# Optimization experiments

Measured on AMD Instinct MI355X. Metric: run time of the kernel, lower is better.

Reference implementation:

```python
import jax, jax.numpy as jnp
import numpy as np

NB, BS = 64, 128          # num_blocks, block_size (W.shape[1]=8192)
TAU = 3.0                 # iteration=0 -> start temperature
SINKHORN_ITERS = 5


def sinkhorn(logits, tau=TAU, iters=SINKHORN_ITERS):
    P = jax.nn.softmax(logits / tau, axis=-1)
    for _ in range(iters):
        P = P / P.sum(axis=-1, keepdims=True)
        P = P / P.sum(axis=-2, keepdims=True)
    return P


def _lsa_min(cost):
    """Hungarian (Jonker-Volgenant / e-maxx) min-cost assignment on a square
    matrix; returns col index for each row. Matches scipy.linear_sum_assignment."""
    cost = np.asarray(cost, np.float64)
    n = cost.shape[0]
    INF = 1e18
    u = np.zeros(n + 1)
    v = np.zeros(n + 1)
    p = np.zeros(n + 1, np.int64)  # p[j] = row (1-based) assigned to column j
    for i in range(1, n + 1):
        p[0] = i
        j0 = 0
        minv = np.full(n + 1, INF)
        used = np.zeros(n + 1, bool)
        way = np.zeros(n + 1, np.int64)
        while True:
            used[j0] = True
            i0 = p[j0]
            free = ~used[1:]
            cur = cost[i0 - 1] - u[i0] - v[1:]
            upd = free & (cur < minv[1:])
            minv[1:][upd] = cur[upd]
            way[1:][upd] = j0
            masked = np.where(free, minv[1:], INF)
            j1 = int(np.argmin(masked)) + 1
            delta = masked[j1 - 1]
            u[p[used]] += delta
            v[used] -= delta
            minv[1:][free] -= delta
            j0 = j1
            if p[j0] == 0:
                break
        while j0 != 0:  # augment along alternating path
            j1 = way[j0]
            p[j0] = p[j1]
            j0 = j1
    col_of_row = np.empty(n, np.int64)
    col_of_row[p[1:] - 1] = np.arange(n)
    return col_of_row


def hungarian_hard(P_np):
    """Per-block hard permutation maximizing P (i.e. min cost = -P)."""
    nb, bs, _ = P_np.shape
    hard = np.zeros((nb, bs, bs), np.float32)
    rows = np.arange(bs)
    for b in range(nb):
        hard[b, rows, _lsa_min(-P_np[b])] = 1.0
    return hard


def _soft_perm(weight, scale):
    w = weight * scale
    # torch: weight.data.clamp_(-1, 1)  -> straight-through clamp
    w = w + jax.lax.stop_gradient(jnp.clip(w, -1.0, 1.0) - w)
    return sinkhorn(w)


def _assemble(blocks):
    nb, bs, _ = blocks.shape
    G = nb * bs
    idx = jnp.arange(nb)
    out = jnp.zeros((nb, bs, nb, bs), blocks.dtype)
    out = out.at[idx, :, idx, :].set(blocks)
    return out.reshape(G, G)


def setup_inputs() -> dict:
    key = jax.random.key(0)
    k1, _ = jax.random.split(key)
    bound = 1.0 / np.sqrt(BS)
    weight = jax.random.uniform(k1, (NB, BS, BS), jnp.float32, -bound, bound)
    scale = jnp.asarray(np.sqrt(BS), jnp.float32)
    return {"weight": weight, "scale": scale}


def reference(weight, scale):
    P = _soft_perm(weight, scale)                       # (NB, BS, BS)
    hard = jnp.asarray(hungarian_hard(np.asarray(P)))   # constant hard perms
    # STE: (hard - P).detach() + P  ==  hard + (P - stop_grad(P))
    blocks = hard + (P - jax.lax.stop_gradient(P))
    return _assemble(blocks)                             # (8192, 8192)
```

## Files before the change

kernel.cpp:

```cpp
#include <hip/hip_runtime.h>
#include <hip/hip_bf16.h>

#define NBLK 64
#define BS   128
#define GSZ  8192

__device__ __forceinline__ int rl32(int v, int sl) {
    return __builtin_amdgcn_readlane(v, sl);
}
__device__ __forceinline__ double rl64(double v, int sl) {
    union { double d; unsigned u[2]; } a; a.d = v;
    unsigned lo = (unsigned)__builtin_amdgcn_readlane((int)a.u[0], sl);
    unsigned hi = (unsigned)__builtin_amdgcn_readlane((int)a.u[1], sl);
    union { unsigned u[2]; double d; } r; r.u[0] = lo; r.u[1] = hi;
    return r.d;
}
__device__ __forceinline__ unsigned long long pkey(double m, int col) {
    union { double d; unsigned long long u; } a; a.d = m;
    unsigned long long x = a.u;
    x = (x >> 63) ? ~x : (x | 0x8000000000000000ull);
    return (x & ~0xFFull) | (unsigned long long)(unsigned)col;
}

__device__ __forceinline__ unsigned wave_min_u32_dpp(unsigned x) {
    x = min(x, (unsigned)__builtin_amdgcn_update_dpp((int)x, (int)x, 0x111, 0xf, 0xf, false));
    x = min(x, (unsigned)__builtin_amdgcn_update_dpp((int)x, (int)x, 0x112, 0xf, 0xf, false));
    x = min(x, (unsigned)__builtin_amdgcn_update_dpp((int)x, (int)x, 0x114, 0xf, 0xf, false));
    x = min(x, (unsigned)__builtin_amdgcn_update_dpp((int)x, (int)x, 0x118, 0xf, 0xf, false));
    x = min(x, (unsigned)__builtin_amdgcn_update_dpp((int)x, (int)x, 0x142, 0xa, 0xf, false));
    x = min(x, (unsigned)__builtin_amdgcn_update_dpp((int)x, (int)x, 0x143, 0xc, 0xf, false));
    return (unsigned)__builtin_amdgcn_readlane((int)x, 63);
}

__device__ __forceinline__ unsigned long long wave_min_key(unsigned long long k) {
    unsigned hi = (unsigned)(k >> 32);
    unsigned lo = (unsigned)k;
    unsigned mh = wave_min_u32_dpp(hi);
    unsigned long long msk = __ballot(hi == mh);
    unsigned lo_cand = (hi == mh) ? lo : 0xFFFFFFFFu;
    unsigned ml;
    if (__popcll(msk) == 1) {
        ml = (unsigned)__builtin_amdgcn_readlane((int)lo_cand, (int)__builtin_ctzll(msk));
    } else {
        ml = wave_min_u32_dpp(lo_cand);
    }
    return ((unsigned long long)mh << 32) | ml;
}

__global__ __launch_bounds__(256) void k_fused(const float* __restrict__ w,
                                               const float* __restrict__ scale_p,
                                               float* __restrict__ out) {
    __shared__ float M[BS][BS + 1];
    __shared__ int   rowasg[BS];
    float* Mf = &M[0][0];

    const int b = blockIdx.x;
    const int t = threadIdx.x;
    const float scale = *scale_p;

    if (t < BS) {
        for (int r = 0; r < BS; ++r) {
            float x = w[((size_t)b * BS + r) * BS + t] * scale;
            x = fminf(fmaxf(x, -1.0f), 1.0f);
            M[r][t] = x / 3.0f;
        }
    }
    __syncthreads();
    if (t < BS) {
        float mx = M[t][0];
        for (int c = 1; c < BS; ++c) mx = fmaxf(mx, M[t][c]);
        float s = 0.0f;
        for (int c = 0; c < BS; ++c) { float e = expf(M[t][c] - mx); M[t][c] = e; s += e; }
        float rs = 1.0f / s;
        for (int c = 0; c < BS; ++c) M[t][c] *= rs;
    }
    __syncthreads();
    for (int it = 0; it < 5; ++it) {
        if (t < BS) {
            float s = 0.0f;
            for (int c = 0; c < BS; ++c) s += M[t][c];
            float rs = 1.0f / s;
            for (int c = 0; c < BS; ++c) M[t][c] *= rs;
        }
        __syncthreads();
        if (t < BS) {
            float s = 0.0f;
            for (int r = 0; r < BS; ++r) s += M[r][t];
            float rs = 1.0f / s;
            for (int r = 0; r < BS; ++r) M[r][t] *= rs;
        }
        __syncthreads();
    }

    int pA = 0, pB = 0;

    if (t >= 64) {
        const int l = t - 64;
        float4 z = make_float4(0.f, 0.f, 0.f, 0.f);
        float4* o4 = reinterpret_cast<float4*>(out + (size_t)b * BS * GSZ);
        for (int k = l; k < BS * GSZ / 4; k += 192) o4[k] = z;
    } else {
        const int jAcol = t + 1, jBcol = t + 65;
        double uA = 0.0, uB = 0.0, vA, vB;

        {
            float cmA = Mf[t];      int raA = 0;
            float cmB = Mf[t + 64]; int raB = 0;
            for (int r = 1; r < BS; ++r) {
                float xA = Mf[r * (BS + 1) + t];
                if (xA > cmA) { cmA = xA; raA = r; }
                float xB = Mf[r * (BS + 1) + t + 64];
                if (xB > cmB) { cmB = xB; raB = r; }
            }
            vA = -(double)cmA; vB = -(double)cmB;
            rowasg[t] = 0x7FFFFFFF; rowasg[t + 64] = 0x7FFFFFFF;
            __threadfence_block();
            atomicMin(&rowasg[raA], jAcol);
            atomicMin(&rowasg[raB], jBcol);
            __threadfence_block();
            pA = (rowasg[raA] == jAcol) ? raA + 1 : 0;
            pB = (rowasg[raB] == jBcol) ? raB + 1 : 0;
        }

        unsigned long long un0 = __ballot(rowasg[t]      == 0x7FFFFFFF);
        unsigned long long un1 = __ballot(rowasg[t + 64] == 0x7FFFFFFF);

        for (int steps = 0; (un0 | un1) && steps < 512; ++steps) {
            int i;
            if (un0) i = __builtin_ctzll(un0) + 1;
            else     i = __builtin_ctzll(un1) + 65;

            double dA = -(double)Mf[(i - 1) * (BS + 1) + t]      - vA;
            double dB = -(double)Mf[(i - 1) * (BS + 1) + t + 64] - vB;
            unsigned long long kA = pkey(dA, jAcol), kB = pkey(dB, jBcol);

            unsigned long long k1 = wave_min_key(kA < kB ? kA : kB);
            const int  j1  = (int)(k1 & 0xFFull);
            const int  sl1 = (j1 - 1) & 63;
            const bool h1  = j1 > 64;
            double u1 = rl64(h1 ? dB : dA, sl1);

            unsigned long long kA2 = (jAcol == j1) ? ~0ull : kA;
            unsigned long long kB2 = (jBcol == j1) ? ~0ull : kB;
            unsigned long long k2 = wave_min_key(kA2 < kB2 ? kA2 : kB2);
            const int  j2  = (int)(k2 & 0xFFull);
            const int  sl2 = (j2 - 1) & 63;
            const bool h2  = j2 > 64;
            double u2 = rl64(h2 ? dB : dA, sl2);

            int i1 = rl32(h1 ? pB : pA, sl1);

            if (t == sl1) {
                if (h1) { pB = i; uB = u2; if (u1 < u2) vB -= (u2 - u1); }
                else    { pA = i; uA = u2; if (u1 < u2) vA -= (u2 - u1); }
            }
            if (i <= 64) un0 &= ~(1ull << (i - 1)); else un1 &= ~(1ull << (i - 65));
            if (i1 > 0) {
                if (i1 <= 64) un0 |= 1ull << (i1 - 1); else un1 |= 1ull << (i1 - 65);
            }
        }

        while (un0 | un1) {
            int i;
            if (un0) { int r = __builtin_ctzll(un0); un0 &= un0 - 1; i = r + 1; }
            else     { int r = __builtin_ctzll(un1); un1 &= un1 - 1; i = r + 65; }

            bool usedA = false, usedB = false;
            double mA = 1e18, mB = 1e18, SUM = 0.0;
            unsigned long long keyA = ~0ull, keyB = ~0ull;
            int wayA = 0, wayB = 0;
            int i0 = i, j0 = 0;
            double ui0 = 0.0;

            for (int guard = 0; guard <= BS + 2; ++guard) {
                float cA = Mf[(i0 - 1) * (BS + 1) + t];
                float cB = Mf[(i0 - 1) * (BS + 1) + t + 64];
                if (!usedA) {
                    double nd = (-(double)cA - ui0 - vA) + SUM;
                    if (nd < mA) { mA = nd; wayA = j0; keyA = pkey(nd, jAcol); }
                }
                if (!usedB) {
                    double nd = (-(double)cB - ui0 - vB) + SUM;
                    if (nd < mB) { mB = nd; wayB = j0; keyB = pkey(nd, jBcol); }
                }
                unsigned long long kw = wave_min_key(keyA < keyB ? keyA : keyB);
                const int  j1 = (int)(kw & 0xFFull);
                const int  sl = (j1 - 1) & 63;
                const bool hb = j1 > 64;

                double m_win = rl64(hb ? mB : mA, sl);
                double delta = m_win - SUM;
                SUM += delta;
                if (usedA) { uA += delta; vA -= delta; }
                if (usedB) { uB += delta; vB -= delta; }

                int pj = rl32(hb ? pB : pA, sl);
                j0 = j1;
                if (pj == 0) break;
                ui0 = rl64(hb ? uB : uA, sl);
                i0 = pj;
                if (!hb && t == sl) { usedA = true; keyA = ~0ull; }
                if ( hb && t == sl) { usedB = true; keyB = ~0ull; }
            }

            int jc = j0;
            for (int guard = 0; guard <= BS + 2; ++guard) {
                const int  slc = (jc - 1) & 63;
                const bool hc  = jc > 64;
                int jp = rl32(hc ? wayB : wayA, slc);
                int nprow; double nu;
                if (jp == 0) { nprow = i; nu = SUM; }
                else {
                    const int  slp = (jp - 1) & 63;
                    const bool hp  = jp > 64;
                    nprow = rl32(hp ? pB : pA, slp);
                    nu    = rl64(hp ? uB : uA, slp);
                }
                if (!hc) { if (t == slc) { pA = nprow; uA = nu; } }
                else     { if (t == slc) { pB = nprow; uB = nu; } }
                if (jp == 0) break;
                jc = jp;
            }
        }
    }

    __syncthreads();

    if (t < 64) {
        const size_t base = (size_t)b * BS;
        if (pA >= 1) out[(base + (size_t)(pA - 1)) * GSZ + base + t]      = 1.0f;
        if (pB >= 1) out[(base + (size_t)(pB - 1)) * GSZ + base + t + 64] = 1.0f;
    }
}

extern "C" void kernel_launch(void* const* d_in, const int* in_sizes, int n_in,
                              void* d_out, int out_size, void* d_ws, size_t ws_size,
                              hipStream_t stream) {
    const float* w     = (const float*)d_in[0];
    const float* scale = (const float*)d_in[1];
    float* out = (float*)d_out;
    k_fused<<<NBLK, 256, 0, stream>>>(w, scale, out);
}
```

Before: 780.3 us.

## Replace auction preprocessing and per-row augmentation with multi-source Dijkstra augmentation

Drops the Jonker-Volgenant-style reduction-transfer preprocessing loop and the single-source-per-row augmentation loop. Each phase now seeds the shortest-path search from all unassigned rows at once (an unrolled-by-4 scan over the unassigned set), finds the nearest free column, and augments back to whichever source row produced it. This is meant to cut wave-wide reductions and dependent readlane chains per augmentation. The cost is an O(unassigned x columns) seeding scan every phase, and the change in tie-breaking could pick a different optimal assignment than the reference when costs tie.

```diff
diff --git a/kernel.cpp b/kernel.cpp
--- a/kernel.cpp
+++ b/kernel.cpp
@@ -125,92 +125,84 @@
         unsigned long long un0 = __ballot(rowasg[t]      == 0x7FFFFFFF);
         unsigned long long un1 = __ballot(rowasg[t + 64] == 0x7FFFFFFF);
 
-        for (int steps = 0; (un0 | un1) && steps < 512; ++steps) {
-            int i;
-            if (un0) i = __builtin_ctzll(un0) + 1;
-            else     i = __builtin_ctzll(un1) + 65;
-
-            double dA = -(double)Mf[(i - 1) * (BS + 1) + t]      - vA;
-            double dB = -(double)Mf[(i - 1) * (BS + 1) + t + 64] - vB;
-            unsigned long long kA = pkey(dA, jAcol), kB = pkey(dB, jBcol);
-
-            unsigned long long k1 = wave_min_key(kA < kB ? kA : kB);
-            const int  j1  = (int)(k1 & 0xFFull);
-            const int  sl1 = (j1 - 1) & 63;
-            const bool h1  = j1 > 64;
-            double u1 = rl64(h1 ? dB : dA, sl1);
-
-            unsigned long long kA2 = (jAcol == j1) ? ~0ull : kA;
-            unsigned long long kB2 = (jBcol == j1) ? ~0ull : kB;
-            unsigned long long k2 = wave_min_key(kA2 < kB2 ? kA2 : kB2);
-            const int  j2  = (int)(k2 & 0xFFull);
-            const int  sl2 = (j2 - 1) & 63;
-            const bool h2  = j2 > 64;
-            double u2 = rl64(h2 ? dB : dA, sl2);
-
-            int i1 = rl32(h1 ? pB : pA, sl1);
-
-            if (t == sl1) {
-                if (h1) { pB = i; uB = u2; if (u1 < u2) vB -= (u2 - u1); }
-                else    { pA = i; uA = u2; if (u1 < u2) vA -= (u2 - u1); }
-            }
-            if (i <= 64) un0 &= ~(1ull << (i - 1)); else un1 &= ~(1ull << (i - 65));
-            if (i1 > 0) {
-                if (i1 <= 64) un0 |= 1ull << (i1 - 1); else un1 |= 1ull << (i1 - 65);
-            }
-        }
-
-        while (un0 | un1) {
-            int i;
-            if (un0) { int r = __builtin_ctzll(un0); un0 &= un0 - 1; i = r + 1; }
-            else     { int r = __builtin_ctzll(un1); un1 &= un1 - 1; i = r + 65; }
+        for (int ph = 0; ph < 132 && (un0 | un1); ++ph) {
+            double mA = 1e18, mB = 1e18;
+            int srcA = 0, srcB = 0, wayA = 0, wayB = 0;
+
+            unsigned long long e0 = un0, e1 = un1;
+            while (e0 | e1) {
+                int r0, r1, r2, r3;
+                if (e0) { r0 = __builtin_ctzll(e0); e0 &= e0 - 1; }
+                else    { r0 = 64 + __builtin_ctzll(e1); e1 &= e1 - 1; }
+                r1 = r0; r2 = r0; r3 = r0;
+                if (e0 | e1) { if (e0) { r1 = __builtin_ctzll(e0); e0 &= e0 - 1; }
+                               else    { r1 = 64 + __builtin_ctzll(e1); e1 &= e1 - 1; } }
+                if (e0 | e1) { if (e0) { r2 = __builtin_ctzll(e0); e0 &= e0 - 1; }
+                               else    { r2 = 64 + __builtin_ctzll(e1); e1 &= e1 - 1; } }
+                if (e0 | e1) { if (e0) { r3 = __builtin_ctzll(e0); e0 &= e0 - 1; }
+                               else    { r3 = 64 + __builtin_ctzll(e1); e1 &= e1 - 1; } }
+                float a0 = Mf[r0 * (BS + 1) + t], b0 = Mf[r0 * (BS + 1) + t + 64];
+                float a1 = Mf[r1 * (BS + 1) + t], b1 = Mf[r1 * (BS + 1) + t + 64];
+                float a2 = Mf[r2 * (BS + 1) + t], b2 = Mf[r2 * (BS + 1) + t + 64];
+                float a3 = Mf[r3 * (BS + 1) + t], b3 = Mf[r3 * (BS + 1) + t + 64];
+                double n0 = -(double)a0 - vA; if (n0 < mA) { mA = n0; srcA = r0 + 1; }
+                double n1 = -(double)a1 - vA; if (n1 < mA) { mA = n1; srcA = r1 + 1; }
+                double n2 = -(double)a2 - vA; if (n2 < mA) { mA = n2; srcA = r2 + 1; }
+                double n3 = -(double)a3 - vA; if (n3 < mA) { mA = n3; srcA = r3 + 1; }
+                double o0 = -(double)b0 - vB; if (o0 < mB) { mB = o0; srcB = r0 + 1; }
+                double o1 = -(double)b1 - vB; if (o1 < mB) { mB = o1; srcB = r1 + 1; }
+                double o2 = -(double)b2 - vB; if (o2 < mB) { mB = o2; srcB = r2 + 1; }
+                double o3 = -(double)b3 - vB; if (o3 < mB) { mB = o3; srcB = r3 + 1; }
+            }
 
             bool usedA = false, usedB = false;
-            double mA = 1e18, mB = 1e18, SUM = 0.0;
-            unsigned long long keyA = ~0ull, keyB = ~0ull;
-            int wayA = 0, wayB = 0;
-            int i0 = i, j0 = 0;
-            double ui0 = 0.0;
-
-            for (int guard = 0; guard <= BS + 2; ++guard) {
+            unsigned long long keyA = pkey(mA, jAcol), keyB = pkey(mB, jBcol);
+            double SUM = 0.0;
+            int jfree = 0;
+
+            for (int guard = 0; guard < BS + 4; ++guard) {
+                unsigned long long kw = wave_min_key(keyA < keyB ? keyA : keyB);
+                const int  j1 = (int)(kw & 0xFFull);
+                const int  sl = (j1 - 1) & 63;
+                const bool hb = j1 > 64;
+
+                double m_win = rl64(hb ? mB : mA, sl);
+                double delta = m_win - SUM;
+                SUM = m_win;
+                if (usedA) { uA += delta; vA -= delta; }
+                if (usedB) { uB += delta; vB -= delta; }
+
+                int pj = rl32(hb ? pB : pA, sl);
+                if (pj == 0) { jfree = j1; break; }
+                double ui0 = rl64(hb ? uB : uA, sl);
+                if (t == sl) { if (hb) { usedB = true; keyB = ~0ull; }
+                               else    { usedA = true; keyA = ~0ull; } }
+                const int i0 = pj;
                 float cA = Mf[(i0 - 1) * (BS + 1) + t];
                 float cB = Mf[(i0 - 1) * (BS + 1) + t + 64];
                 if (!usedA) {
                     double nd = (-(double)cA - ui0 - vA) + SUM;
-                    if (nd < mA) { mA = nd; wayA = j0; keyA = pkey(nd, jAcol); }
+                    if (nd < mA) { mA = nd; wayA = j1; keyA = pkey(nd, jAcol); }
                 }
                 if (!usedB) {
                     double nd = (-(double)cB - ui0 - vB) + SUM;
-                    if (nd < mB) { mB = nd; wayB = j0; keyB = pkey(nd, jBcol); }
+                    if (nd < mB) { mB = nd; wayB = j1; keyB = pkey(nd, jBcol); }
                 }
-                unsigned long long kw = wave_min_key(keyA < keyB ? keyA : keyB);
-                const int  j1 = (int)(kw & 0xFFull);
-                const int  sl = (j1 - 1) & 63;
-                const bool hb = j1 > 64;
-
-                double m_win = rl64(hb ? mB : mA, sl);
-                double delta = m_win - SUM;
-                SUM += delta;
-                if (usedA) { uA += delta; vA -= delta; }
-                if (usedB) { uB += delta; vB -= delta; }
-
-                int pj = rl32(hb ? pB : pA, sl);
-                j0 = j1;
-                if (pj == 0) break;
-                ui0 = rl64(hb ? uB : uA, sl);
-                i0 = pj;
-                if (!hb && t == sl) { usedA = true; keyA = ~0ull; }
-                if ( hb && t == sl) { usedB = true; keyB = ~0ull; }
-            }
-
-            int jc = j0;
-            for (int guard = 0; guard <= BS + 2; ++guard) {
+            }
+
+            if (!jfree) break;
+
+            int isrc = 0;
+            int jc = jfree;
+            for (int guard = 0; guard < BS + 4; ++guard) {
                 const int  slc = (jc - 1) & 63;
                 const bool hc  = jc > 64;
                 int jp = rl32(hc ? wayB : wayA, slc);
                 int nprow; double nu;
-                if (jp == 0) { nprow = i; nu = SUM; }
-                else {
+                if (jp == 0) {
+                    isrc = rl32(hc ? srcB : srcA, slc);
+                    nprow = isrc; nu = SUM;
+                } else {
                     const int  slp = (jp - 1) & 63;
                     const bool hp  = jp > 64;
                     nprow = rl32(hp ? pB : pA, slp);
@@ -221,6 +213,10 @@
                 if (jp == 0) break;
                 jc = jp;
             }
+            if (isrc >= 1) {
+                if (isrc <= 64) un0 &= ~(1ull << (isrc - 1));
+                else            un1 &= ~(1ull << (isrc - 65));
+            } else break;
         }
     }
 
```

Measured after the change: 1.580 ms. 102% more time.

## Replace serial auction warmup with parallel bidding rounds and pack assignment into key

Applied to the files above, without the earlier changes.

Replaces the serial per-row auction-style initialization with parallel bidding rounds: every free row scans all columns for its best and second-best reduced cost, then bids via shared-memory atomicMax, and winners update prices and assignments. Rounds stop after a fixed cap or when progress stalls. The Dijkstra phase now packs the column's assigned row into the reduction key, which drops a readlane, and it exits early when every key is exhausted. This aims to cut the number of serial augmenting steps, at the cost of a full 128-column scan per round and a bid priority that is quantized to float precision.

```diff
diff --git a/kernel.cpp b/kernel.cpp
--- a/kernel.cpp
+++ b/kernel.cpp
@@ -15,11 +15,12 @@
     union { unsigned u[2]; double d; } r; r.u[0] = lo; r.u[1] = hi;
     return r.d;
 }
-__device__ __forceinline__ unsigned long long pkey(double m, int col) {
+__device__ __forceinline__ unsigned long long pkey16(double m, int pj, int col) {
     union { double d; unsigned long long u; } a; a.d = m;
     unsigned long long x = a.u;
     x = (x >> 63) ? ~x : (x | 0x8000000000000000ull);
-    return (x & ~0xFFull) | (unsigned long long)(unsigned)col;
+    return (x & ~0xFFFFull) | ((unsigned long long)(unsigned)pj << 8)
+                            | (unsigned long long)(unsigned)col;
 }
 
 __device__ __forceinline__ unsigned wave_min_u32_dpp(unsigned x) {
@@ -31,7 +32,6 @@
     x = min(x, (unsigned)__builtin_amdgcn_update_dpp((int)x, (int)x, 0x143, 0xc, 0xf, false));
     return (unsigned)__builtin_amdgcn_readlane((int)x, 63);
 }
-
 __device__ __forceinline__ unsigned long long wave_min_key(unsigned long long k) {
     unsigned hi = (unsigned)(k >> 32);
     unsigned lo = (unsigned)k;
@@ -50,8 +50,13 @@
 __global__ __launch_bounds__(256) void k_fused(const float* __restrict__ w,
                                                const float* __restrict__ scale_p,
                                                float* __restrict__ out) {
-    __shared__ float M[BS][BS + 1];
-    __shared__ int   rowasg[BS];
+    __shared__ float    M[BS][BS + 1];
+    __shared__ int      rowasg[BS];
+    __shared__ double   vldS[BS];
+    __shared__ unsigned bidS[BS];
+    __shared__ int      wrowS[BS];
+    __shared__ double   wu2S[BS];
+    __shared__ double   wduS[BS];
     float* Mf = &M[0][0];
 
     const int b = blockIdx.x;
@@ -125,38 +130,60 @@
         unsigned long long un0 = __ballot(rowasg[t]      == 0x7FFFFFFF);
         unsigned long long un1 = __ballot(rowasg[t + 64] == 0x7FFFFFFF);
 
-        for (int steps = 0; (un0 | un1) && steps < 512; ++steps) {
-            int i;
-            if (un0) i = __builtin_ctzll(un0) + 1;
-            else     i = __builtin_ctzll(un1) + 65;
-
-            double dA = -(double)Mf[(i - 1) * (BS + 1) + t]      - vA;
-            double dB = -(double)Mf[(i - 1) * (BS + 1) + t + 64] - vB;
-            unsigned long long kA = pkey(dA, jAcol), kB = pkey(dB, jBcol);
-
-            unsigned long long k1 = wave_min_key(kA < kB ? kA : kB);
-            const int  j1  = (int)(k1 & 0xFFull);
-            const int  sl1 = (j1 - 1) & 63;
-            const bool h1  = j1 > 64;
-            double u1 = rl64(h1 ? dB : dA, sl1);
-
-            unsigned long long kA2 = (jAcol == j1) ? ~0ull : kA;
-            unsigned long long kB2 = (jBcol == j1) ? ~0ull : kB;
-            unsigned long long k2 = wave_min_key(kA2 < kB2 ? kA2 : kB2);
-            const int  j2  = (int)(k2 & 0xFFull);
-            const int  sl2 = (j2 - 1) & 63;
-            const bool h2  = j2 > 64;
-            double u2 = rl64(h2 ? dB : dA, sl2);
-
-            int i1 = rl32(h1 ? pB : pA, sl1);
-
-            if (t == sl1) {
-                if (h1) { pB = i; uB = u2; if (u1 < u2) vB -= (u2 - u1); }
-                else    { pA = i; uA = u2; if (u1 < u2) vA -= (u2 - u1); }
-            }
-            if (i <= 64) un0 &= ~(1ull << (i - 1)); else un1 &= ~(1ull << (i - 65));
-            if (i1 > 0) {
-                if (i1 <= 64) un0 |= 1ull << (i1 - 1); else un1 |= 1ull << (i1 - 65);
+        {
+            volatile double*   vl   = vldS;
+            volatile unsigned* bidv = bidS;
+            volatile int*      wrow = wrowS;
+            volatile double*   wu2  = wu2S;
+            volatile double*   wdu  = wduS;
+            volatile int*      asg  = rowasg;
+            int stall = 0;
+            for (int rd = 0; rd < 24 && (un0 | un1); ++rd) {
+                vl[t] = vA; vl[t + 64] = vB;
+                bidv[t] = 0u; bidv[t + 64] = 0u;
+                wrow[t] = 0;  wrow[t + 64] = 0;
+                const bool fA = (un0 >> t) & 1ull;
+                const bool fB = (un1 >> t) & 1ull;
+                double u1A = 1e18, u2A = 1e18, u1B = 1e18, u2B = 1e18;
+                int j1A = 1, j1B = 1;
+                for (int c = 0; c < BS; ++c) {
+                    double vv = vl[c];
+                    float  a  = Mf[t * (BS + 1) + c];
+                    float  bq = Mf[(t + 64) * (BS + 1) + c];
+                    double da = -(double)a  - vv;
+                    double db = -(double)bq - vv;
+                    if (fA) { if (da < u1A) { u2A = u1A; u1A = da; j1A = c + 1; }
+                              else if (da < u2A) u2A = da; }
+                    if (fB) { if (db < u1B) { u2B = u1B; u1B = db; j1B = c + 1; }
+                              else if (db < u2B) u2B = db; }
+                }
+                unsigned pkA = 0, pkB = 0;
+                if (fA) { unsigned ib = __float_as_uint((float)(u2A - u1A));
+                          pkA = (((ib >> 7) + 1u) << 7) | (unsigned)t;
+                          atomicMax(&bidS[j1A - 1], pkA); }
+                if (fB) { unsigned ib = __float_as_uint((float)(u2B - u1B));
+                          pkB = (((ib >> 7) + 1u) << 7) | (unsigned)(t + 64);
+                          atomicMax(&bidS[j1B - 1], pkB); }
+                if (fA && bidv[j1A - 1] == pkA) {
+                    wrow[j1A - 1] = t + 1;  wu2[j1A - 1] = u2A; wdu[j1A - 1] = u2A - u1A;
+                }
+                if (fB && bidv[j1B - 1] == pkB) {
+                    wrow[j1B - 1] = t + 65; wu2[j1B - 1] = u2B; wdu[j1B - 1] = u2B - u1B;
+                }
+                { int wa = wrow[t];
+                  if (wa > 0) { pA = wa; uA = wu2[t];      vA -= wdu[t]; } }
+                { int wb = wrow[t + 64];
+                  if (wb > 0) { pB = wb; uB = wu2[t + 64]; vB -= wdu[t + 64]; } }
+                asg[t] = 0; asg[t + 64] = 0;
+                if (pA > 0) asg[pA - 1] = 1;
+                if (pB > 0) asg[pB - 1] = 1;
+                unsigned long long n0 = __ballot(asg[t] == 0);
+                unsigned long long n1 = __ballot(asg[t + 64] == 0);
+                int oldf = __popcll(un0) + __popcll(un1);
+                int newf = __popcll(n0) + __popcll(n1);
+                un0 = n0; un1 = n1;
+                if (newf < oldf) stall = 0;
+                else if (++stall >= 2) break;
             }
         }
 
@@ -173,34 +200,35 @@
             double ui0 = 0.0;
 
             for (int guard = 0; guard <= BS + 2; ++guard) {
-                float cA = Mf[(i0 - 1) * (BS + 1) + t];
-                float cB = Mf[(i0 - 1) * (BS + 1) + t + 64];
+                float cAv = Mf[(i0 - 1) * (BS + 1) + t];
+                float cBv = Mf[(i0 - 1) * (BS + 1) + t + 64];
                 if (!usedA) {
-                    double nd = (-(double)cA - ui0 - vA) + SUM;
-                    if (nd < mA) { mA = nd; wayA = j0; keyA = pkey(nd, jAcol); }
+                    double nd = (-(double)cAv - ui0 - vA) + SUM;
+                    if (nd < mA) { mA = nd; wayA = j0; keyA = pkey16(nd, pA, jAcol); }
                 }
                 if (!usedB) {
-                    double nd = (-(double)cB - ui0 - vB) + SUM;
-                    if (nd < mB) { mB = nd; wayB = j0; keyB = pkey(nd, jBcol); }
+                    double nd = (-(double)cBv - ui0 - vB) + SUM;
+                    if (nd < mB) { mB = nd; wayB = j0; keyB = pkey16(nd, pB, jBcol); }
                 }
                 unsigned long long kw = wave_min_key(keyA < keyB ? keyA : keyB);
+                if (kw == ~0ull) break;
                 const int  j1 = (int)(kw & 0xFFull);
+                const int  pj = (int)((kw >> 8) & 0xFFull);
                 const int  sl = (j1 - 1) & 63;
                 const bool hb = j1 > 64;
 
                 double m_win = rl64(hb ? mB : mA, sl);
                 double delta = m_win - SUM;
-                SUM += delta;
+                SUM = m_win;
                 if (usedA) { uA += delta; vA -= delta; }
                 if (usedB) { uB += delta; vB -= delta; }
 
-                int pj = rl32(hb ? pB : pA, sl);
                 j0 = j1;
                 if (pj == 0) break;
                 ui0 = rl64(hb ? uB : uA, sl);
                 i0 = pj;
-                if (!hb && t == sl) { usedA = true; keyA = ~0ull; }
-                if ( hb && t == sl) { usedB = true; keyB = ~0ull; }
+                if (t == sl) { if (hb) { usedB = true; keyB = ~0ull; }
+                               else    { usedA = true; keyA = ~0ull; } }
             }
 
             int jc = j0;
```

Result: slower. 837.9 us (+7.4%).
